# Optimization experiments

Measured on AMD Instinct MI355X. Metric: run time of the kernel, lower is better.

## Reference

```python
import jax, jax.numpy as jnp
import numpy as np

RCUT, RCUT_SMTH = 6.0, 0.5
SEL = [32, 64]
SEC = [0, 32, 96]
PAIRS = [(0, 0), (0, 1), (1, 1)]  # (ti, tj) with ti <= tj, matching stacked weight index
NF, NLOC, NALL = 1, 256, 512
NNEI = sum(SEL)
NG = 96


def setup_inputs() -> dict:
    key = jax.random.key(0)
    ks = jax.random.split(key, 10)
    # coords in a 4A cube so most neighbor distances are inside rcut=6
    extended_coord = jax.random.uniform(ks[0], (NF, NALL * 3), dtype=jnp.float32) * 4.0
    nl = jax.random.randint(ks[1], (NF, NLOC, NNEI), 0, NALL - 1)
    # shift indices >= own local index by 1 to avoid self-neighbors (zero distance)
    nlist = nl + (nl >= jnp.arange(NLOC)[None, :, None]).astype(nl.dtype)
    extended_atype = jax.random.randint(ks[2], (NF, NALL), 0, 2)
    mean = jnp.zeros((2, NNEI, 4), jnp.float32)
    stddev = jnp.ones((2, NNEI, 4), jnp.float32)
    def w(k, shape, fan):
        return jax.random.normal(k, shape, jnp.float32) / np.float32(np.sqrt(fan))
    W1 = w(ks[3], (3, 1, 24), 1.0)
    b1 = 0.1 * jax.random.normal(ks[4], (3, 24), jnp.float32)
    W2 = w(ks[5], (3, 24, 48), 24.0)
    b2 = 0.1 * jax.random.normal(ks[6], (3, 48), jnp.float32)
    W3 = w(ks[7], (3, 48, 96), 48.0)
    b3 = 0.1 * jax.random.normal(ks[8], (3, 96), jnp.float32)
    return dict(nlist=nlist, extended_coord=extended_coord, extended_atype=extended_atype,
                mean=mean, stddev=stddev, W1=W1, b1=b1, W2=W2, b2=b2, W3=W3, b3=b3)


def _smooth_weight(r, rmin, rmax):
    uu = (r - rmin) / (rmax - rmin)
    vv = uu * uu * uu * (-6.0 * uu * uu + 15.0 * uu - 10.0) + 1.0
    return jnp.where(r <= rmin, 1.0, jnp.where(r >= rmax, 0.0, vv))


def _env_mat(nlist, coord, atype, mean, stddev):
    nf, nloc, nnei = nlist.shape
    coord = coord.reshape(nf, -1, 3)
    mask = nlist >= 0
    nl = jnp.where(mask, nlist, 0)
    # gather neighbor coords: nf x nloc x nnei x 3
    coord_r = jnp.take_along_axis(coord, nl.reshape(nf, -1, 1), axis=1).reshape(nf, nloc, nnei, 3)
    diff = coord_r - coord[:, :nloc, None, :]
    length = jnp.linalg.norm(diff, axis=-1, keepdims=True)
    length = length + (~mask)[..., None].astype(diff.dtype)  # avoid 0-div on padded entries
    t0 = 1.0 / length
    t1 = diff / (length * length)
    sw = _smooth_weight(length, RCUT_SMTH, RCUT) * mask[..., None].astype(diff.dtype)
    env = jnp.concatenate([t0, t1], axis=-1) * sw  # nf x nloc x nnei x 4
    loc_type = atype[:, :nloc]
    dmatrix = (env - mean[loc_type]) / stddev[loc_type]
    return dmatrix, sw


def _embed(x, W1, b1, W2, b2, W3, b3):
    # EmbeddingNet 1->24->48->96, tanh, resnet doubling residuals
    h1 = jnp.tanh(x @ W1 + b1)
    h2 = jnp.tanh(h1 @ W2 + b2) + jnp.concatenate([h1, h1], axis=-1)
    h3 = jnp.tanh(h2 @ W3 + b3) + jnp.concatenate([h2, h2], axis=-1)
    return h3


def reference(nlist, extended_coord, extended_atype, mean, stddev, W1, b1, W2, b2, W3, b3):
    nf, nloc, nnei = nlist.shape
    dmatrix, sw = _env_mat(nlist, extended_coord, extended_atype, mean, stddev)
    dm = dmatrix.reshape(nf * nloc, nnei, 4)
    result = jnp.zeros((nf * nloc, NG), dm.dtype)
    for p, (ti, tj) in enumerate(PAIRS):
        rr_i = dm[:, SEC[ti]:SEC[ti + 1], 1:]  # nfnl x nt_i x 3
        rr_j = dm[:, SEC[tj]:SEC[tj + 1], 1:]  # nfnl x nt_j x 3
        env_ij = jnp.einsum('ijm,ikm->ijk', rr_i, rr_j)  # nfnl x nt_i x nt_j
        gg = _embed(env_ij[..., None], W1[p], b1[p], W2[p], b2[p], W3[p], b3[p])
        res_ij = jnp.einsum('ijk,ijkm->im', env_ij, gg)
        result = result + res_ij * (1.0 / (SEL[ti] * SEL[tj]))
    return result.reshape(nf, nloc, NG)
```

## Files before the change

kernel.cpp:

```cpp
#include <hip/hip_runtime.h>

#define NLOC 256
#define NNEI 96
#define NG   96
#define H1W  28
#define H2W  52
#define TWO_LOG2E 2.88539008177793f

typedef __attribute__((ext_vector_type(8))) short short8;
typedef __attribute__((ext_vector_type(4))) float f32x4;
union Frag { uint4 u; short8 s; };

__device__ __forceinline__ float tanh_sc(float s) {
    float e = __builtin_amdgcn_exp2f(s);
    return 1.0f - 2.0f * __builtin_amdgcn_rcpf(e + 1.0f);
}
__device__ __forceinline__ unsigned short f2bf(float f) {
    unsigned int u = __float_as_uint(f);
    u += 0x7FFFu + ((u >> 16) & 1u);
    return (unsigned short)(u >> 16);
}
__device__ __forceinline__ unsigned short f2bf_rhu(float f) {
    return (unsigned short)((__float_as_uint(f) + 0x8000u) >> 16);
}
__device__ __forceinline__ unsigned int pack_bf2(float lo, float hi) {
    unsigned int a = __float_as_uint(lo) + 0x8000u;
    unsigned int b = __float_as_uint(hi) + 0x8000u;
    return __builtin_amdgcn_perm(b, a, 0x07060302);
}

__global__ __launch_bounds__(256) void prep_kernel(
        const float* __restrict__ W1, const float* __restrict__ b1,
        const float* __restrict__ W2, const float* __restrict__ b2,
        const float* __restrict__ W3, const float* __restrict__ b3,
        unsigned short* __restrict__ wf2, unsigned short* __restrict__ wf3,
        unsigned short* __restrict__ wfJ,
        float* __restrict__ w1s, float* __restrict__ b1s,
        float* __restrict__ b2s, float* __restrict__ b3s,
        float* __restrict__ out) {
    int t = blockIdx.x * blockDim.x + threadIdx.x;
    if (t < NLOC * NG) out[t] = 0.0f;
    if (t < 2880) {
        int p = t / 960;
        int r = t % 960;
        int tile = r / 64;
        int l = r % 64;
        int nlo = l & 15, g = l >> 4;
        short8 v;
        if (tile < 3) {
            int nt = tile;
            #pragma unroll
            for (int j = 0; j < 8; j++) {
                int k = g * 8 + j;
                float w = (k < 24) ? W2[(p * 24 + k) * 48 + nt * 16 + nlo] * TWO_LOG2E : 0.0f;
                v[j] = (short)f2bf(w);
            }
            *(short8*)(wf2 + ((p * 3 + nt) * 64 + l) * 8) = v;
        } else {
            int tt = tile - 3;
            int nt = tt >> 1, kc = tt & 1;
            #pragma unroll
            for (int j = 0; j < 8; j++) {
                int kk = (kc == 0) ? (g * 8 + j) : ((j < 4) ? (32 + g * 4 + j) : -1);
                float w = (kk >= 0) ? W3[(p * 48 + kk) * 96 + nt * 16 + nlo] * TWO_LOG2E : 0.0f;
                v[j] = (short)f2bf(w);
            }
            *(short8*)(wf3 + ((p * 12 + nt * 2 + kc) * 64 + l) * 8) = v;
        }
    } else if (t < 3264) {
        int t2 = t - 2880;
        int f = t2 >> 6, l = t2 & 63;
        int ml = l & 15, g = l >> 4;
        short8 v;
        if (f < 3) {
            int c24 = (f * 16 + ml) % 24;
            #pragma unroll
            for (int j = 0; j < 8; j++)
                v[j] = (short)((g * 8 + j == c24) ? 0x3F80 : 0);
        } else {
            int nt2 = f - 3;
            if (nt2 < 2) {
                int c = nt2 * 16 + ml;
                #pragma unroll
                for (int j = 0; j < 8; j++)
                    v[j] = (short)((g * 8 + j == c) ? 0x3F80 : 0);
            } else {
                #pragma unroll
                for (int j = 0; j < 8; j++)
                    v[j] = (short)((j < 4 && (g * 4 + j) == ml) ? 0x3F80 : 0);
            }
        }
        *(short8*)(wfJ + (f * 64 + l) * 8) = v;
    } else if (t < 3768) {
        int u = t - 3264;
        if (u < 72)       { w1s[u] = W1[u] * TWO_LOG2E; b1s[u] = b1[u] * TWO_LOG2E; }
        else if (u < 216) { b2s[u - 72]  = b2[u - 72]  * TWO_LOG2E; }
        else              { b3s[u - 216] = b3[u - 216] * TWO_LOG2E; }
    }
}

__launch_bounds__(256, 4)
__global__ void mlp_kernel(const int* __restrict__ nlist, const float* __restrict__ coord,
                           const int* __restrict__ atype,
                           const float* __restrict__ mean, const float* __restrict__ stddev,
                           const float* __restrict__ w1s, const float* __restrict__ b1s,
                           const float* __restrict__ b2s, const float* __restrict__ b3s,
                           const unsigned short* __restrict__ wf2,
                           const unsigned short* __restrict__ wf3,
                           const unsigned short* __restrict__ wfJ,
                           float* __restrict__ out) {
    __shared__ __align__(16) unsigned char smem[40960];
    unsigned short* h1s = (unsigned short*)smem;
    unsigned short* h2s = (unsigned short*)(smem + 14336);
    float* rrl = (float*)(smem + 39808);
    unsigned char* h2b = (unsigned char*)h2s;

    int tid = threadIdx.x;
    int blk = blockIdx.x;
    int i = blk / 28;
    int b = blk % 28;
    int p, base_e, offi, offj, lgnj;
    float scale;
    if (b < 4)       { p = 0; base_e = b * 256;        offi = 0;  offj = 0;  lgnj = 5; scale = 1.0f/1024.0f; }
    else if (b < 12) { p = 1; base_e = (b - 4) * 256;  offi = 0;  offj = 32; lgnj = 6; scale = 1.0f/2048.0f; }
    else             { p = 2; base_e = (b - 12) * 256; offi = 32; offj = 32; lgnj = 6; scale = 1.0f/4096.0f; }

    if (tid < NNEI) {
        int n = tid;
        int idx = nlist[i * NNEI + n];
        bool msk = idx >= 0;
        int safe = msk ? idx : 0;
        float cx = coord[i*3], cy = coord[i*3+1], cz = coord[i*3+2];
        float dx = coord[safe*3]   - cx;
        float dy = coord[safe*3+1] - cy;
        float dz = coord[safe*3+2] - cz;
        float rn = sqrtf(dx*dx + dy*dy + dz*dz) + (msk ? 0.0f : 1.0f);
        float sw;
        if (rn <= 0.5f)      sw = 1.0f;
        else if (rn >= 6.0f) sw = 0.0f;
        else {
            float uu = (rn - 0.5f) * (1.0f / 5.5f);
            sw = uu*uu*uu*(uu*(-6.0f*uu + 15.0f) - 10.0f) + 1.0f;
        }
        if (!msk) sw = 0.0f;
        float ir2 = 1.0f / (rn * rn);
        int ty = atype[i];
        const float* mu = mean   + (ty * NNEI + n) * 4;
        const float* sd = stddev + (ty * NNEI + n) * 4;
        rrl[n*3+0] = (dx * ir2 * sw - mu[1]) / sd[1];
        rrl[n*3+1] = (dy * ir2 * sw - mu[2]) / sd[2];
        rrl[n*3+2] = (dz * ir2 * sw - mu[3]) / sd[3];
    }
    __syncthreads();

    float x;
    {
        int e = base_e + tid;
        int jj = e >> lgnj;
        int kk = e & ((1 << lgnj) - 1);
        const float* ri = rrl + (offi + jj) * 3;
        const float* rj = rrl + (offj + kk) * 3;
        x = ri[0]*rj[0] + ri[1]*rj[1] + ri[2]*rj[2];
        const float* w1 = w1s + p * 24;
        const float* c1 = b1s + p * 24;
        float h1v[24];
        #pragma unroll
        for (int u = 0; u < 24; u++)
            h1v[u] = tanh_sc(fmaf(x, w1[u], c1[u]));
        #pragma unroll
        for (int t4 = 0; t4 < 6; t4++) {
            uint2 q = { pack_bf2(h1v[4*t4], h1v[4*t4+1]),
                        pack_bf2(h1v[4*t4+2], h1v[4*t4+3]) };
            *(uint2*)(h1s + tid*H1W + 4*t4) = q;
        }
        uint2 z2 = {0u, 0u};
        *(uint2*)(h1s + tid*H1W + 24) = z2;
        if (tid == 0) *(uint2*)h2s = z2;
    }
    __syncthreads();

    *(float*)(h2b + tid*104 + 96) = x;
    if (tid < NG) *(float*)(h2b + tid*104 + 100) = 0.0f;

    int l  = tid & 63;
    int w  = tid >> 6;
    int ml = l & 15, g = l >> 4;

    short8 bw2[3], jf2[3];
    float  b2c[3];
    #pragma unroll
    for (int nt = 0; nt < 3; nt++) {
        bw2[nt] = *(const short8*)(wf2 + ((p*3 + nt)*64 + l)*8);
        jf2[nt] = *(const short8*)(wfJ + (nt*64 + l)*8);
        b2c[nt] = b2s[p*48 + nt*16 + ml];
    }
    #pragma unroll
    for (int mi = 0; mi < 4; mi++) {
        int mt = w*4 + mi;
        int arow = mt*16 + ml;
        uint2 lo = *(const uint2*)(h1s + arow*H1W + g*8);
        uint2 hi = *(const uint2*)(h1s + arow*H1W + g*8 + 4);
        Frag fa; fa.u = make_uint4(lo.x, lo.y, hi.x, hi.y);
        #pragma unroll
        for (int nt = 0; nt < 3; nt++) {
            f32x4 bini = {b2c[nt], b2c[nt], b2c[nt], b2c[nt]};
            f32x4 zz   = {0.f, 0.f, 0.f, 0.f};
            f32x4 acc = __builtin_amdgcn_mfma_f32_16x16x32_bf16(fa.s, bw2[nt], bini, 0, 0, 0);
            f32x4 aj  = __builtin_amdgcn_mfma_f32_16x16x32_bf16(fa.s, jf2[nt], zz,   0, 0, 0);
            int col = nt*16 + ml;
            #pragma unroll
            for (int r = 0; r < 4; r++) {
                int orow = mt*16 + g*4 + r;
                float v = tanh_sc(acc[r]) + aj[r];
                h2s[orow*H2W + col] = f2bf_rhu(v);
            }
        }
    }
    __syncthreads();

    short8 a3a[4], a3b[4];
    float  xv[4][4];
    #pragma unroll
    for (int mi = 0; mi < 4; mi++) {
        int mt = w*4 + mi;
        int arow = mt*16 + ml;
        uint2 lo = *(const uint2*)(h2s + arow*H2W + g*8);
        uint2 hi = *(const uint2*)(h2s + arow*H2W + g*8 + 4);
        Frag fa; fa.u = make_uint4(lo.x, lo.y, hi.x, hi.y);
        a3a[mi] = fa.s;
        uint2 t2 = *(const uint2*)(h2s + arow*H2W + 32 + g*4);
        Frag fb; fb.u = make_uint4(t2.x, t2.y, 0u, 0u);
        a3b[mi] = fb.s;
        #pragma unroll
        for (int r = 0; r < 4; r++)
            xv[mi][r] = *(const float*)(h2b + (mt*16 + g*4 + r)*104 + 96);
    }
    short8 jf3[3];
    #pragma unroll
    for (int q = 0; q < 3; q++)
        jf3[q] = *(const short8*)(wfJ + ((3 + q)*64 + l)*8);

    #pragma unroll
    for (int nt2 = 0; nt2 < 3; nt2++) {
        f32x4 zz = {0.f, 0.f, 0.f, 0.f};
        f32x4 aj[4];
        #pragma unroll
        for (int mi = 0; mi < 4; mi++)
            aj[mi] = __builtin_amdgcn_mfma_f32_16x16x32_bf16(
                (nt2 == 2) ? a3b[mi] : a3a[mi], jf3[nt2], zz, 0, 0, 0);
        #pragma unroll
        for (int h = 0; h < 2; h++) {
            int nt = nt2 + 3*h;
            short8 b30 = *(const short8*)(wf3 + ((p*12 + nt*2 + 0)*64 + l)*8);
            short8 b31 = *(const short8*)(wf3 + ((p*12 + nt*2 + 1)*64 + l)*8);
            float b3c = b3s[p*96 + nt*16 + ml];
            float facc = 0.0f;
            #pragma unroll
            for (int mi = 0; mi < 4; mi++) {
                f32x4 bini = {b3c, b3c, b3c, b3c};
                f32x4 acc = __builtin_amdgcn_mfma_f32_16x16x32_bf16(a3a[mi], b30, bini, 0, 0, 0);
                acc = __builtin_amdgcn_mfma_f32_16x16x32_bf16(a3b[mi], b31, acc, 0, 0, 0);
                #pragma unroll
                for (int r = 0; r < 4; r++) {
                    float h3 = tanh_sc(acc[r]) + aj[mi][r];
                    facc += xv[mi][r] * h3;
                }
            }
            facc += __shfl_xor(facc, 16, 64);
            facc += __shfl_xor(facc, 32, 64);
            if (g == 0) atomicAdd((float*)(h2b + (nt*16 + ml)*104 + 100), facc);
        }
    }
    __syncthreads();
    if (tid < NG)
        atomicAdd(&out[i*NG + tid], *(const float*)(h2b + tid*104 + 100) * scale);
}

extern "C" void kernel_launch(void* const* d_in, const int* in_sizes, int n_in,
                              void* d_out, int out_size, void* d_ws, size_t ws_size,
                              hipStream_t stream) {
    const int*   nlist  = (const int*)  d_in[0];
    const float* coord  = (const float*)d_in[1];
    const int*   atype  = (const int*)  d_in[2];
    const float* mean   = (const float*)d_in[3];
    const float* stddev = (const float*)d_in[4];
    const float* W1     = (const float*)d_in[5];
    const float* b1     = (const float*)d_in[6];
    const float* W2     = (const float*)d_in[7];
    const float* b2     = (const float*)d_in[8];
    const float* W3     = (const float*)d_in[9];
    const float* b3     = (const float*)d_in[10];
    float* out = (float*)d_out;

    char* ws = (char*)d_ws;
    unsigned short* wf2 = (unsigned short*)(ws + 0);
    unsigned short* wf3 = (unsigned short*)(ws + 9216);
    unsigned short* wfJ = (unsigned short*)(ws + 46080);
    float* w1s = (float*)(ws + 52224);
    float* b1s = (float*)(ws + 52512);
    float* b2s = (float*)(ws + 52800);
    float* b3s = (float*)(ws + 53376);

    prep_kernel<<<96, 256, 0, stream>>>(W1, b1, W2, b2, W3, b3,
                                        wf2, wf3, wfJ, w1s, b1s, b2s, b3s, out);
    mlp_kernel<<<NLOC * 28, 256, 0, stream>>>(
        nlist, coord, atype, mean, stddev,
        w1s, b1s, b2s, b3s, wf2, wf3, wfJ, out);
}
```

Before: 164.4 us.

## Exploit symmetry of same-type pair blocks and fold weight prep into main kernel

For the same-type pairs (0,0) and (1,1) the env matrix is symmetric, so only the upper triangle is computed, with off-diagonal entries weighted by two. This cuts the grid from 28 to 20 blocks per atom. The separate prep kernel is removed: bf16 weight fragments and identity fragments are built in registers inside the main kernel from the raw fp32 weights, and the output is zeroed with a memset. The trade-off is redundant per-block weight loads and conversions, plus triangular index math that uses a float sqrt.

```diff
diff --git a/kernel.cpp b/kernel.cpp
--- a/kernel.cpp
+++ b/kernel.cpp
@@ -5,7 +5,7 @@
 #define NG   96
 #define H1W  28
 #define H2W  52
-#define TWO_LOG2E 2.88539008177793f
+#define S2LE 2.88539008177793f
 
 typedef __attribute__((ext_vector_type(8))) short short8;
 typedef __attribute__((ext_vector_type(4))) float f32x4;
@@ -14,11 +14,6 @@
 __device__ __forceinline__ float tanh_sc(float s) {
     float e = __builtin_amdgcn_exp2f(s);
     return 1.0f - 2.0f * __builtin_amdgcn_rcpf(e + 1.0f);
-}
-__device__ __forceinline__ unsigned short f2bf(float f) {
-    unsigned int u = __float_as_uint(f);
-    u += 0x7FFFu + ((u >> 16) & 1u);
-    return (unsigned short)(u >> 16);
 }
 __device__ __forceinline__ unsigned short f2bf_rhu(float f) {
     return (unsigned short)((__float_as_uint(f) + 0x8000u) >> 16);
@@ -29,86 +24,14 @@
     return __builtin_amdgcn_perm(b, a, 0x07060302);
 }
 
-__global__ __launch_bounds__(256) void prep_kernel(
-        const float* __restrict__ W1, const float* __restrict__ b1,
-        const float* __restrict__ W2, const float* __restrict__ b2,
-        const float* __restrict__ W3, const float* __restrict__ b3,
-        unsigned short* __restrict__ wf2, unsigned short* __restrict__ wf3,
-        unsigned short* __restrict__ wfJ,
-        float* __restrict__ w1s, float* __restrict__ b1s,
-        float* __restrict__ b2s, float* __restrict__ b3s,
-        float* __restrict__ out) {
-    int t = blockIdx.x * blockDim.x + threadIdx.x;
-    if (t < NLOC * NG) out[t] = 0.0f;
-    if (t < 2880) {
-        int p = t / 960;
-        int r = t % 960;
-        int tile = r / 64;
-        int l = r % 64;
-        int nlo = l & 15, g = l >> 4;
-        short8 v;
-        if (tile < 3) {
-            int nt = tile;
-            #pragma unroll
-            for (int j = 0; j < 8; j++) {
-                int k = g * 8 + j;
-                float w = (k < 24) ? W2[(p * 24 + k) * 48 + nt * 16 + nlo] * TWO_LOG2E : 0.0f;
-                v[j] = (short)f2bf(w);
-            }
-            *(short8*)(wf2 + ((p * 3 + nt) * 64 + l) * 8) = v;
-        } else {
-            int tt = tile - 3;
-            int nt = tt >> 1, kc = tt & 1;
-            #pragma unroll
-            for (int j = 0; j < 8; j++) {
-                int kk = (kc == 0) ? (g * 8 + j) : ((j < 4) ? (32 + g * 4 + j) : -1);
-                float w = (kk >= 0) ? W3[(p * 48 + kk) * 96 + nt * 16 + nlo] * TWO_LOG2E : 0.0f;
-                v[j] = (short)f2bf(w);
-            }
-            *(short8*)(wf3 + ((p * 12 + nt * 2 + kc) * 64 + l) * 8) = v;
-        }
-    } else if (t < 3264) {
-        int t2 = t - 2880;
-        int f = t2 >> 6, l = t2 & 63;
-        int ml = l & 15, g = l >> 4;
-        short8 v;
-        if (f < 3) {
-            int c24 = (f * 16 + ml) % 24;
-            #pragma unroll
-            for (int j = 0; j < 8; j++)
-                v[j] = (short)((g * 8 + j == c24) ? 0x3F80 : 0);
-        } else {
-            int nt2 = f - 3;
-            if (nt2 < 2) {
-                int c = nt2 * 16 + ml;
-                #pragma unroll
-                for (int j = 0; j < 8; j++)
-                    v[j] = (short)((g * 8 + j == c) ? 0x3F80 : 0);
-            } else {
-                #pragma unroll
-                for (int j = 0; j < 8; j++)
-                    v[j] = (short)((j < 4 && (g * 4 + j) == ml) ? 0x3F80 : 0);
-            }
-        }
-        *(short8*)(wfJ + (f * 64 + l) * 8) = v;
-    } else if (t < 3768) {
-        int u = t - 3264;
-        if (u < 72)       { w1s[u] = W1[u] * TWO_LOG2E; b1s[u] = b1[u] * TWO_LOG2E; }
-        else if (u < 216) { b2s[u - 72]  = b2[u - 72]  * TWO_LOG2E; }
-        else              { b3s[u - 216] = b3[u - 216] * TWO_LOG2E; }
-    }
-}
-
 __launch_bounds__(256, 4)
-__global__ void mlp_kernel(const int* __restrict__ nlist, const float* __restrict__ coord,
-                           const int* __restrict__ atype,
-                           const float* __restrict__ mean, const float* __restrict__ stddev,
-                           const float* __restrict__ w1s, const float* __restrict__ b1s,
-                           const float* __restrict__ b2s, const float* __restrict__ b3s,
-                           const unsigned short* __restrict__ wf2,
-                           const unsigned short* __restrict__ wf3,
-                           const unsigned short* __restrict__ wfJ,
-                           float* __restrict__ out) {
+__global__ void fused_kernel(const int* __restrict__ nlist, const float* __restrict__ coord,
+                             const int* __restrict__ atype,
+                             const float* __restrict__ mean, const float* __restrict__ stddev,
+                             const float* __restrict__ W1, const float* __restrict__ b1,
+                             const float* __restrict__ W2, const float* __restrict__ b2,
+                             const float* __restrict__ W3, const float* __restrict__ b3,
+                             float* __restrict__ out) {
     __shared__ __align__(16) unsigned char smem[40960];
     unsigned short* h1s = (unsigned short*)smem;
     unsigned short* h2s = (unsigned short*)(smem + 14336);
@@ -117,13 +40,15 @@
 
     int tid = threadIdx.x;
     int blk = blockIdx.x;
-    int i = blk / 28;
-    int b = blk % 28;
-    int p, base_e, offi, offj, lgnj;
+    int i = blk / 20;
+    int b = blk - i * 20;
+
+    int p, base_e, offi, offj, count, Aint;
     float scale;
-    if (b < 4)       { p = 0; base_e = b * 256;        offi = 0;  offj = 0;  lgnj = 5; scale = 1.0f/1024.0f; }
-    else if (b < 12) { p = 1; base_e = (b - 4) * 256;  offi = 0;  offj = 32; lgnj = 6; scale = 1.0f/2048.0f; }
-    else             { p = 2; base_e = (b - 12) * 256; offi = 32; offj = 32; lgnj = 6; scale = 1.0f/4096.0f; }
+    bool tri;
+    if (b < 3)       { p=0; base_e=b*256;      offi=0;  offj=0;  scale=1.0f/1024.0f; count=528;  tri=true;  Aint=65;  }
+    else if (b < 11) { p=1; base_e=(b-3)*256;  offi=0;  offj=32; scale=1.0f/2048.0f; count=2048; tri=false; Aint=0;   }
+    else             { p=2; base_e=(b-11)*256; offi=32; offj=32; scale=1.0f/4096.0f; count=2080; tri=true;  Aint=129; }
 
     if (tid < NNEI) {
         int n = tid;
@@ -153,20 +78,36 @@
     }
     __syncthreads();
 
-    float x;
+    float xs;
     {
         int e = base_e + tid;
-        int jj = e >> lgnj;
-        int kk = e & ((1 << lgnj) - 1);
+        bool valid = e < count;
+        int ec = valid ? e : 0;
+        int jj, kk;
+        float mult = 1.0f;
+        if (!tri) { jj = ec >> 6; kk = ec & 63; }
+        else {
+            float Af = (float)Aint;
+            int j = (int)((Af - sqrtf(Af*Af - 8.0f*(float)ec)) * 0.5f);
+            int Tj1 = ((j+1)*(Aint-j-1)) >> 1;
+            if (ec >= Tj1) j++;
+            int Tj = (j*(Aint-j)) >> 1;
+            if (ec < Tj) { j--; Tj = (j*(Aint-j)) >> 1; }
+            jj = j; kk = j + (ec - Tj);
+            mult = (jj == kk) ? 1.0f : 2.0f;
+        }
         const float* ri = rrl + (offi + jj) * 3;
         const float* rj = rrl + (offj + kk) * 3;
-        x = ri[0]*rj[0] + ri[1]*rj[1] + ri[2]*rj[2];
-        const float* w1 = w1s + p * 24;
-        const float* c1 = b1s + p * 24;
+        float x = ri[0]*rj[0] + ri[1]*rj[1] + ri[2]*rj[2];
+        x = valid ? x : 0.0f;
+        xs = x * mult;
+
+        const float* w1 = W1 + p * 24;
+        const float* c1 = b1 + p * 24;
         float h1v[24];
         #pragma unroll
         for (int u = 0; u < 24; u++)
-            h1v[u] = tanh_sc(fmaf(x, w1[u], c1[u]));
+            h1v[u] = tanh_sc(fmaf(x, w1[u], c1[u]) * S2LE);
         #pragma unroll
         for (int t4 = 0; t4 < 6; t4++) {
             uint2 q = { pack_bf2(h1v[4*t4], h1v[4*t4+1]),
@@ -175,11 +116,10 @@
         }
         uint2 z2 = {0u, 0u};
         *(uint2*)(h1s + tid*H1W + 24) = z2;
-        if (tid == 0) *(uint2*)h2s = z2;
-    }
-    __syncthreads();
-
-    *(float*)(h2b + tid*104 + 96) = x;
+    }
+    __syncthreads();
+
+    *(float*)(h2b + tid*104 + 96) = xs;
     if (tid < NG) *(float*)(h2b + tid*104 + 100) = 0.0f;
 
     int l  = tid & 63;
@@ -190,10 +130,24 @@
     float  b2c[3];
     #pragma unroll
     for (int nt = 0; nt < 3; nt++) {
-        bw2[nt] = *(const short8*)(wf2 + ((p*3 + nt)*64 + l)*8);
-        jf2[nt] = *(const short8*)(wfJ + (nt*64 + l)*8);
-        b2c[nt] = b2s[p*48 + nt*16 + ml];
-    }
+        Frag f;
+        #pragma unroll
+        for (int j2 = 0; j2 < 4; j2++) {
+            int k0 = g*8 + 2*j2;
+            float wa = (k0     < 24) ? W2[(p*24 + k0    )*48 + nt*16 + ml] * S2LE : 0.0f;
+            float wb = (k0 + 1 < 24) ? W2[(p*24 + k0 + 1)*48 + nt*16 + ml] * S2LE : 0.0f;
+            ((unsigned int*)&f.u)[j2] = pack_bf2(wa, wb);
+        }
+        bw2[nt] = f.s;
+        int c24 = nt*16 + ml; if (c24 >= 24) c24 -= 24;
+        short8 jv;
+        #pragma unroll
+        for (int j3 = 0; j3 < 8; j3++)
+            jv[j3] = (short)((g*8 + j3 == c24) ? 0x3F80 : 0);
+        jf2[nt] = jv;
+        b2c[nt] = b2[p*48 + nt*16 + ml] * S2LE;
+    }
+
     #pragma unroll
     for (int mi = 0; mi < 4; mi++) {
         int mt = w*4 + mi;
@@ -237,8 +191,20 @@
     }
     short8 jf3[3];
     #pragma unroll
-    for (int q = 0; q < 3; q++)
-        jf3[q] = *(const short8*)(wfJ + ((3 + q)*64 + l)*8);
+    for (int q = 0; q < 3; q++) {
+        short8 jv;
+        if (q < 2) {
+            int c = q*16 + ml;
+            #pragma unroll
+            for (int j3 = 0; j3 < 8; j3++)
+                jv[j3] = (short)((g*8 + j3 == c) ? 0x3F80 : 0);
+        } else {
+            #pragma unroll
+            for (int j3 = 0; j3 < 8; j3++)
+                jv[j3] = (short)((j3 < 4 && (g*4 + j3) == ml) ? 0x3F80 : 0);
+        }
+        jf3[q] = jv;
+    }
 
     #pragma unroll
     for (int nt2 = 0; nt2 < 3; nt2++) {
@@ -251,15 +217,29 @@
         #pragma unroll
         for (int h = 0; h < 2; h++) {
             int nt = nt2 + 3*h;
-            short8 b30 = *(const short8*)(wf3 + ((p*12 + nt*2 + 0)*64 + l)*8);
-            short8 b31 = *(const short8*)(wf3 + ((p*12 + nt*2 + 1)*64 + l)*8);
-            float b3c = b3s[p*96 + nt*16 + ml];
+            Frag f0, f1;
+            #pragma unroll
+            for (int j2 = 0; j2 < 4; j2++) {
+                int k0 = g*8 + 2*j2;
+                float wa = W3[(p*48 + k0    )*96 + nt*16 + ml] * S2LE;
+                float wb = W3[(p*48 + k0 + 1)*96 + nt*16 + ml] * S2LE;
+                ((unsigned int*)&f0.u)[j2] = pack_bf2(wa, wb);
+            }
+            #pragma unroll
+            for (int j2 = 0; j2 < 2; j2++) {
+                int k0 = 32 + g*4 + 2*j2;
+                float wa = W3[(p*48 + k0    )*96 + nt*16 + ml] * S2LE;
+                float wb = W3[(p*48 + k0 + 1)*96 + nt*16 + ml] * S2LE;
+                ((unsigned int*)&f1.u)[j2] = pack_bf2(wa, wb);
+            }
+            f1.u.z = 0u; f1.u.w = 0u;
+            float b3c = b3[p*96 + nt*16 + ml] * S2LE;
             float facc = 0.0f;
             #pragma unroll
             for (int mi = 0; mi < 4; mi++) {
                 f32x4 bini = {b3c, b3c, b3c, b3c};
-                f32x4 acc = __builtin_amdgcn_mfma_f32_16x16x32_bf16(a3a[mi], b30, bini, 0, 0, 0);
-                acc = __builtin_amdgcn_mfma_f32_16x16x32_bf16(a3b[mi], b31, acc, 0, 0, 0);
+                f32x4 acc = __builtin_amdgcn_mfma_f32_16x16x32_bf16(a3a[mi], f0.s, bini, 0, 0, 0);
+                acc = __builtin_amdgcn_mfma_f32_16x16x32_bf16(a3b[mi], f1.s, acc, 0, 0, 0);
                 #pragma unroll
                 for (int r = 0; r < 4; r++) {
                     float h3 = tanh_sc(acc[r]) + aj[mi][r];
@@ -292,18 +272,7 @@
     const float* b3     = (const float*)d_in[10];
     float* out = (float*)d_out;
 
-    char* ws = (char*)d_ws;
-    unsigned short* wf2 = (unsigned short*)(ws + 0);
-    unsigned short* wf3 = (unsigned short*)(ws + 9216);
-    unsigned short* wfJ = (unsigned short*)(ws + 46080);
-    float* w1s = (float*)(ws + 52224);
-    float* b1s = (float*)(ws + 52512);
-    float* b2s = (float*)(ws + 52800);
-    float* b3s = (float*)(ws + 53376);
-
-    prep_kernel<<<96, 256, 0, stream>>>(W1, b1, W2, b2, W3, b3,
-                                        wf2, wf3, wfJ, w1s, b1s, b2s, b3s, out);
-    mlp_kernel<<<NLOC * 28, 256, 0, stream>>>(
-        nlist, coord, atype, mean, stddev,
-        w1s, b1s, b2s, b3s, wf2, wf3, wfJ, out);
-}
+    hipMemsetAsync(out, 0, (size_t)out_size * sizeof(float), stream);
+    fused_kernel<<<NLOC * 20, 256, 0, stream>>>(
+        nlist, coord, atype, mean, stddev, W1, b1, W2, b2, W3, b3, out);
+}
```

Result: faster. 153.5 us (-6.6%).
